# Kernel tuning notes

Hardware: AMD Instinct MI355X
Metric: run time of the kernel (lower is better)

## Reference

```python
import jax, jax.numpy as jnp
import numpy as np

B, S, V, D, L, H = 2, 512, 100300, 768, 12, 3072


def setup_inputs() -> dict:
    key = jax.random.key(0)
    ks = jax.random.split(key, 24)
    nrm = lambda k, shape, s=0.02: (jax.random.normal(k, shape, jnp.float32) * s)
    uni = lambda k, shape: jax.random.uniform(k, shape, jnp.float32)
    return {
        "tokens": jax.random.randint(ks[0], (B, S), 0, V, dtype=jnp.int32),
        "emb": nrm(ks[1], (V, D)),
        "ln0_g": jnp.ones((D,), jnp.float32), "ln0_b": jnp.zeros((D,), jnp.float32),
        "ln1_g": jnp.ones((L, D), jnp.float32), "ln1_b": jnp.zeros((L, D), jnp.float32),
        "ln2_g": jnp.ones((L, D), jnp.float32), "ln2_b": jnp.zeros((L, D), jnp.float32),
        "time_decay": nrm(ks[2], (L, D), 0.5),
        "time_first": nrm(ks[3], (L, D), 0.5),
        "tm_mu_k": uni(ks[4], (L, D)), "tm_mu_v": uni(ks[5], (L, D)), "tm_mu_r": uni(ks[6], (L, D)),
        "tm_Wk": nrm(ks[7], (L, D, D)), "tm_Wv": nrm(ks[8], (L, D, D)),
        "tm_Wr": nrm(ks[9], (L, D, D)), "tm_Wo": nrm(ks[10], (L, D, D)),
        "cm_mu_k": uni(ks[11], (L, D)), "cm_mu_r": uni(ks[12], (L, D)),
        "cm_Wk": nrm(ks[13], (L, D, H)), "cm_Wv": nrm(ks[14], (L, H, D)), "cm_Wr": nrm(ks[15], (L, D, D)),
        "lnf_g": jnp.ones((D,), jnp.float32), "lnf_b": jnp.zeros((D,), jnp.float32),
        "head": nrm(ks[16], (D, V)),
    }


def _ln(x, g, b, eps=1e-5):
    m = jnp.mean(x, axis=-1, keepdims=True)
    v = jnp.mean(jnp.square(x - m), axis=-1, keepdims=True)
    return (x - m) * jax.lax.rsqrt(v + eps) * g + b


def _shift(x):  # previous-token shift along seq axis, zeros at t=0; x: [B,S,D]
    return jnp.concatenate([jnp.zeros_like(x[:, :1]), x[:, :-1]], axis=1)


def _wkv(k, v, w, u):
    """RWKV-4 max-stabilized WKV linear recurrence. k,v: [B,S,D]; w,u: [D]."""
    decay = -jnp.exp(w)  # negative per-channel decay

    def step(carry, inp):
        p, a, b = carry
        kt, vt = inp
        ww = u + kt
        q = jnp.maximum(p, ww)
        e1 = jnp.exp(p - q)
        e2 = jnp.exp(ww - q)
        out = (e1 * a + e2 * vt) / (e1 * b + e2)
        ww2 = p + decay
        q2 = jnp.maximum(ww2, kt)
        e1 = jnp.exp(ww2 - q2)
        e2 = jnp.exp(kt - q2)
        return (q2, e1 * a + e2 * vt, e1 * b + e2), out

    kT = jnp.swapaxes(k, 0, 1)  # [S,B,D]
    vT = jnp.swapaxes(v, 0, 1)
    p0 = jnp.full((k.shape[0], k.shape[2]), -1e38, k.dtype)
    a0 = jnp.zeros_like(p0)
    b0 = jnp.zeros_like(p0)
    _, out = jax.lax.scan(step, (p0, a0, b0), (kT, vT))
    return jnp.swapaxes(out, 0, 1)  # [B,S,D]


def reference(tokens, emb, ln0_g, ln0_b, ln1_g, ln1_b, ln2_g, ln2_b,
              time_decay, time_first, tm_mu_k, tm_mu_v, tm_mu_r,
              tm_Wk, tm_Wv, tm_Wr, tm_Wo, cm_mu_k, cm_mu_r,
              cm_Wk, cm_Wv, cm_Wr, lnf_g, lnf_b, head):
    x = emb[tokens]                      # [B,S,D]
    x = _ln(x, ln0_g, ln0_b)
    n_layer = ln1_g.shape[0]
    for l in range(n_layer):
        # --- time mixing ---
        xx = _ln(x, ln1_g[l], ln1_b[l])
        sx = _shift(xx)
        xk = xx * tm_mu_k[l] + sx * (1.0 - tm_mu_k[l])
        xv = xx * tm_mu_v[l] + sx * (1.0 - tm_mu_v[l])
        xr = xx * tm_mu_r[l] + sx * (1.0 - tm_mu_r[l])
        r = jax.nn.sigmoid(jnp.einsum('bsd,de->bse', xr, tm_Wr[l]))
        k = jnp.einsum('bsd,de->bse', xk, tm_Wk[l])
        v = jnp.einsum('bsd,de->bse', xv, tm_Wv[l])
        wkv = _wkv(k, v, time_decay[l], time_first[l])
        x = x + jnp.einsum('bsd,de->bse', r * wkv, tm_Wo[l])
        # --- channel mixing ---
        xx = _ln(x, ln2_g[l], ln2_b[l])
        sx = _shift(xx)
        xk = xx * cm_mu_k[l] + sx * (1.0 - cm_mu_k[l])
        xr = xx * cm_mu_r[l] + sx * (1.0 - cm_mu_r[l])
        kk = jnp.square(jax.nn.relu(jnp.einsum('bsd,dh->bsh', xk, cm_Wk[l])))
        x = x + jax.nn.sigmoid(jnp.einsum('bsd,de->bse', xr, cm_Wr[l])) * jnp.einsum('bsh,hd->bsd', kk, cm_Wv[l])
    x = _ln(x, lnf_g, lnf_b)
    return jnp.einsum('bsd,dv->bsv', x, head)  # [B,S,V] logits
```

## Files before the change

### kernel.cpp

```cpp
#include <hip/hip_runtime.h>

typedef float f32x4v __attribute__((ext_vector_type(4)));
typedef __bf16 bf16x8 __attribute__((ext_vector_type(8)));

__device__ __forceinline__ ushort f2bf(float f) {
    unsigned u = __builtin_bit_cast(unsigned, f);
    return (ushort)((u + 0x7FFFu + ((u >> 16) & 1u)) >> 16);
}

__device__ __forceinline__ void gload16(const void* g, void* l) {
    __builtin_amdgcn_global_load_lds(
        (const __attribute__((address_space(1))) void*)g,
        (__attribute__((address_space(3))) void*)l, 16, 0, 0);
}

__global__ __launch_bounds__(256)
void prep_w(const float* __restrict__ Win, ushort* __restrict__ Wout,
            int K, int N, size_t sIn, size_t sOut)
{
    __shared__ float t[64][65];
    const float* W = Win + sIn * blockIdx.z;
    ushort* O = Wout + sOut * blockIdx.z;
    int n0 = blockIdx.x * 64, k0 = blockIdx.y * 64;
    int tid = threadIdx.x;
    int c = tid & 63, r4 = tid >> 6;
#pragma unroll
    for (int i = 0; i < 16; i++) {
        int rr = i * 4 + r4;
        int n = n0 + c;
        t[rr][c] = (n < N) ? W[(size_t)(k0 + rr) * N + n] : 0.f;
    }
    __syncthreads();
#pragma unroll
    for (int i = 0; i < 16; i++) {
        int nr = i * 4 + r4;
        O[(size_t)(n0 + nr) * K + k0 + c] = f2bf(t[c][nr]);
    }
}

__global__ __launch_bounds__(256)
void prep_dd(const float* __restrict__ W0, const float* __restrict__ W1,
             const float* __restrict__ W2, const float* __restrict__ W3,
             const float* __restrict__ W4,
             ushort* __restrict__ O0, ushort* __restrict__ O1,
             ushort* __restrict__ O2, ushort* __restrict__ O3,
             ushort* __restrict__ O4)
{
    __shared__ float t[64][65];
    const int z = blockIdx.z, wsel = z / 12, l = z % 12;
    const size_t DD = (size_t)768 * 768;
    const float* W = (wsel == 0 ? W0 : wsel == 1 ? W1 : wsel == 2 ? W2 : wsel == 3 ? W3 : W4) + DD * l;
    ushort* O = (wsel == 0 ? O0 : wsel == 1 ? O1 : wsel == 2 ? O2 : wsel == 3 ? O3 : O4) + DD * l;
    int n0 = blockIdx.x * 64, k0 = blockIdx.y * 64;
    int tid = threadIdx.x;
    int c = tid & 63, r4 = tid >> 6;
#pragma unroll
    for (int i = 0; i < 16; i++) {
        int rr = i * 4 + r4;
        t[rr][c] = W[(size_t)(k0 + rr) * 768 + n0 + c];
    }
    __syncthreads();
#pragma unroll
    for (int i = 0; i < 16; i++) {
        int nr = i * 4 + r4;
        O[(size_t)(n0 + nr) * 768 + k0 + c] = f2bf(t[c][nr]);
    }
}

template <int BM, int BN, int EPI>
__device__ __forceinline__
void gemm_body(const ushort* __restrict__ A, const ushort* __restrict__ B,
               float* __restrict__ C, ushort* __restrict__ Obf,
               const float* __restrict__ G,
               int N, int K, int mtiles, int bid, int tid,
               ushort* __restrict__ As, ushort* __restrict__ Bs)
{
    constexpr int WM = BM / 2, WN = BN / 2, MF = WM / 16, NF = WN / 16;
    const int mt = bid % mtiles, nt = bid / mtiles;
    const int m0 = mt * BM, n0 = nt * BN;
    const int w = tid >> 6, l = tid & 63;
    const int wr = w >> 1, wc = w & 1, g = l >> 4, lr = l & 15;
    const int lrow = l >> 3, lcol = ((l & 7) ^ lrow) * 8;

    auto stage = [&](int buf, int k0) {
#pragma unroll
        for (int i = 0; i < BM / 32; i++) {
            int rb = (i * 4 + w) * 8;
            gload16(A + (size_t)(m0 + rb + lrow) * K + k0 + lcol, &As[buf * BM * 64 + rb * 64]);
        }
#pragma unroll
        for (int i = 0; i < BN / 32; i++) {
            int rb = (i * 4 + w) * 8;
            gload16(B + (size_t)(n0 + rb + lrow) * K + k0 + lcol, &Bs[buf * BN * 64 + rb * 64]);
        }
    };

    f32x4v acc[MF][NF] = {};
    auto comp = [&](int buf) {
#pragma unroll
        for (int kk = 0; kk < 2; kk++) {
            bf16x8 af[MF], bfr[NF];
            const int sl = ((kk * 4 + g) ^ (lr & 7)) * 8;
#pragma unroll
            for (int mi = 0; mi < MF; mi++)
                af[mi] = *(const bf16x8*)&As[buf * BM * 64 + (wr * WM + mi * 16 + lr) * 64 + sl];
#pragma unroll
            for (int ni = 0; ni < NF; ni++)
                bfr[ni] = *(const bf16x8*)&Bs[buf * BN * 64 + (wc * WN + ni * 16 + lr) * 64 + sl];
#pragma unroll
            for (int mi = 0; mi < MF; mi++)
#pragma unroll
                for (int ni = 0; ni < NF; ni++)
                    acc[mi][ni] = __builtin_amdgcn_mfma_f32_16x16x32_bf16(
                        af[mi], bfr[ni], acc[mi][ni], 0, 0, 0);
        }
    };

    const int NS = K >> 6;
    stage(0, 0);
    __syncthreads();
    for (int s = 0; s < NS; s++) {
        if (s + 1 < NS) stage((s + 1) & 1, (s + 1) << 6);
        comp(s & 1);
        __syncthreads();
    }

#pragma unroll
    for (int mi = 0; mi < MF; mi++) {
        int row = m0 + wr * WM + mi * 16 + 4 * g;
#pragma unroll
        for (int ni = 0; ni < NF; ni++) {
            int col = n0 + wc * WN + ni * 16 + lr;
#pragma unroll
            for (int q = 0; q < 4; q++) {
                size_t idx = (size_t)(row + q) * N + col;
                float vv = acc[mi][ni][q];
                if constexpr (EPI == 0) {
                    C[idx] = vv;
                } else if constexpr (EPI == 1) {
                    C[idx] += vv;
                } else if constexpr (EPI == 2) {
                    float t = vv > 0.f ? vv : 0.f;
                    Obf[idx] = f2bf(t * t);
                } else {
                    float gt = 1.f / (1.f + __expf(-G[idx]));
                    C[idx] += gt * vv;
                }
            }
        }
    }
}

template <int BM, int BN, int EPI>
__global__ __launch_bounds__(256)
void gemm2(const ushort* __restrict__ Abase,
           const ushort* __restrict__ B0, const ushort* __restrict__ B1,
           const ushort* __restrict__ B2,
           float* __restrict__ Cbase, ushort* __restrict__ ObfBase,
           const float* __restrict__ Gbase,
           int M, int N, int K, int mtiles)
{
    __shared__ ushort As[2 * BM * 64];
    __shared__ ushort Bs[2 * BN * 64];
    const int z = blockIdx.z;
    const ushort* A = Abase + (size_t)z * M * K;
    const ushort* B = (z == 0) ? B0 : ((z == 1) ? B1 : B2);
    float* C = Cbase ? Cbase + (size_t)z * M * N : nullptr;
    ushort* Obf = ObfBase ? ObfBase + (size_t)z * M * N : nullptr;
    int bid = blockIdx.x;
    { int cpx = gridDim.x >> 3; bid = (bid & 7) * cpx + (bid >> 3); }
    gemm_body<BM, BN, EPI>(A, B, C, Obf, Gbase, N, K, mtiles, bid, threadIdx.x, As, Bs);
}

__global__ __launch_bounds__(256)
void gemm_ckcr(const ushort* __restrict__ xk, const ushort* __restrict__ xr,
               const ushort* __restrict__ ckT, const ushort* __restrict__ crT,
               ushort* __restrict__ hbuf, float* __restrict__ rrb)
{
    __shared__ ushort As[2 * 64 * 64];
    __shared__ ushort Bs[2 * 128 * 64];
    int bid = blockIdx.x;
    { int cpx = gridDim.x >> 3; bid = (bid & 7) * cpx + (bid >> 3); }
    if (bid < 384)
        gemm_body<64, 128, 2>(xk, ckT, nullptr, hbuf, nullptr, 3072, 768, 16,
                              bid, threadIdx.x, As, Bs);
    else
        gemm_body<64, 64, 0>(xr, crT, rrb, nullptr, nullptr, 768, 768, 16,
                             bid - 384, threadIdx.x, As, Bs);
}

__global__ __launch_bounds__(256, 4)
void head_gemm(const ushort* __restrict__ A, const ushort* __restrict__ B,
               float* __restrict__ C, int M, int N, int K, int mtiles)
{
    constexpr int WM = 64, WN = 64;
    __shared__ ushort As[2][128 * 32];
    __shared__ ushort Bs[2][128 * 32];

    int bid = blockIdx.x;
    { int cpx = gridDim.x >> 3; bid = (bid & 7) * cpx + (bid >> 3); }
    const int mt = bid % mtiles, nt = bid / mtiles;
    const int m0 = mt * 128, n0 = nt * 128;
    const int tid = threadIdx.x, w = tid >> 6, l = tid & 63;
    const int wr = w >> 1, wc = w & 1, g = l >> 4, lr = l & 15;
    const int lrow = l >> 2;
    const int lcol = ((l & 3) ^ (lrow & 3) ^ ((lrow >> 2) & 3)) * 8;

    auto stage = [&](int buf, int k0) {
#pragma unroll
        for (int i = 0; i < 2; i++) {
            int rg = i * 4 + w;
            gload16(A + (size_t)(m0 + rg * 16 + lrow) * K + k0 + lcol, &As[buf][rg * 512]);
        }
#pragma unroll
        for (int i = 0; i < 2; i++) {
            int rg = i * 4 + w;
            gload16(B + (size_t)(n0 + rg * 16 + lrow) * K + k0 + lcol, &Bs[buf][rg * 512]);
        }
    };

    f32x4v acc[4][4] = {};
    auto comp = [&](int buf) {
        bf16x8 af[4], bfr[4];
        const int sl = (g ^ (lr & 3) ^ ((lr >> 2) & 3)) * 8;
#pragma unroll
        for (int mi = 0; mi < 4; mi++)
            af[mi] = *(const bf16x8*)&As[buf][(wr * WM + mi * 16 + lr) * 32 + sl];
#pragma unroll
        for (int ni = 0; ni < 4; ni++)
            bfr[ni] = *(const bf16x8*)&Bs[buf][(wc * WN + ni * 16 + lr) * 32 + sl];
#pragma unroll
        for (int mi = 0; mi < 4; mi++)
#pragma unroll
            for (int ni = 0; ni < 4; ni++)
                acc[mi][ni] = __builtin_amdgcn_mfma_f32_16x16x32_bf16(
                    af[mi], bfr[ni], acc[mi][ni], 0, 0, 0);
    };

    const int NS = K / 32;
    stage(0, 0);
    __syncthreads();
    for (int s = 0; s < NS; s++) {
        if (s + 1 < NS) stage((s + 1) & 1, (s + 1) * 32);
        comp(s & 1);
        __syncthreads();
    }

#pragma unroll
    for (int mi = 0; mi < 4; mi++) {
        int row = m0 + wr * WM + mi * 16 + 4 * g;
#pragma unroll
        for (int ni = 0; ni < 4; ni++) {
            int col = n0 + wc * WN + ni * 16 + lr;
            if (col >= N) continue;
#pragma unroll
            for (int q = 0; q < 4; q++)
                C[(size_t)(row + q) * N + col] = acc[mi][ni][q];
        }
    }
}

__device__ __forceinline__ float4 blockReduce4(float4 v) {
#pragma unroll
    for (int off = 32; off; off >>= 1) {
        v.x += __shfl_down(v.x, off);
        v.y += __shfl_down(v.y, off);
        v.z += __shfl_down(v.z, off);
        v.w += __shfl_down(v.w, off);
    }
    __shared__ float4 red[4];
    int tid = threadIdx.x;
    if ((tid & 63) == 0) red[tid >> 6] = v;
    __syncthreads();
    float4 r = red[0];
    r.x += red[1].x + red[2].x + red[3].x;
    r.y += red[1].y + red[2].y + red[3].y;
    r.z += red[1].z + red[2].z + red[3].z;
    r.w += red[1].w + red[2].w + red[3].w;
    return r;
}

__global__ void embed_ln0(const int* __restrict__ tokens, const float* __restrict__ emb,
                          const float* __restrict__ g, const float* __restrict__ be,
                          float* __restrict__ x)
{
    int tau = blockIdx.x, tid = threadIdx.x;
    const float* e = emb + (size_t)tokens[tau] * 768;
    float a[3]; float s1 = 0, s2 = 0;
#pragma unroll
    for (int i = 0; i < 3; i++) {
        float av = e[tid + i * 256]; a[i] = av; s1 += av; s2 += av * av;
    }
    float4 r = blockReduce4(make_float4(s1, s2, 0.f, 0.f));
    const float inv = 1.f / 768.f;
    float m = r.x * inv, va = r.y * inv - m * m, rs = rsqrtf(va + 1e-5f);
#pragma unroll
    for (int i = 0; i < 3; i++) {
        int d = tid + i * 256;
        x[(size_t)tau * 768 + d] = (a[i] - m) * rs * g[d] + be[d];
    }
}

__global__ void ln_mix_tm(const float* __restrict__ x,
                          const float* __restrict__ g, const float* __restrict__ be,
                          const float* __restrict__ muk, const float* __restrict__ muv,
                          const float* __restrict__ mur,
                          ushort* __restrict__ xk, ushort* __restrict__ xv,
                          ushort* __restrict__ xr)
{
    int tau = blockIdx.x, tid = threadIdx.x;
    bool hasp = (tau & 511) != 0;
    const float* xp = x + (size_t)tau * 768;
    const float* pp = xp - 768;
    float a[3], b[3]; float s1 = 0, s2 = 0, s3 = 0, s4 = 0;
#pragma unroll
    for (int i = 0; i < 3; i++) {
        int d = tid + i * 256;
        float av = xp[d]; a[i] = av; s1 += av; s2 += av * av;
        float bv = hasp ? pp[d] : 0.f; b[i] = bv; s3 += bv; s4 += bv * bv;
    }
    float4 r = blockReduce4(make_float4(s1, s2, s3, s4));
    const float inv = 1.f / 768.f;
    float m1 = r.x * inv, va = r.y * inv - m1 * m1, rs1 = rsqrtf(va + 1e-5f);
    float m2 = r.z * inv, vb = r.w * inv - m2 * m2, rs2 = rsqrtf(vb + 1e-5f);
#pragma unroll
    for (int i = 0; i < 3; i++) {
        int d = tid + i * 256;
        float gg = g[d], bb = be[d];
        float xx = (a[i] - m1) * rs1 * gg + bb;
        float sx = hasp ? ((b[i] - m2) * rs2 * gg + bb) : 0.f;
        size_t o = (size_t)tau * 768 + d;
        float mk = muk[d]; xk[o] = f2bf(xx * mk + sx * (1.f - mk));
        float mv = muv[d]; xv[o] = f2bf(xx * mv + sx * (1.f - mv));
        float mr = mur[d]; xr[o] = f2bf(xx * mr + sx * (1.f - mr));
    }
}

__global__ void ln_mix_cm(const float* __restrict__ x,
                          const float* __restrict__ g, const float* __restrict__ be,
                          const float* __restrict__ muk, const float* __restrict__ mur,
                          ushort* __restrict__ xk, ushort* __restrict__ xr)
{
    int tau = blockIdx.x, tid = threadIdx.x;
    bool hasp = (tau & 511) != 0;
    const float* xp = x + (size_t)tau * 768;
    const float* pp = xp - 768;
    float a[3], b[3]; float s1 = 0, s2 = 0, s3 = 0, s4 = 0;
#pragma unroll
    for (int i = 0; i < 3; i++) {
        int d = tid + i * 256;
        float av = xp[d]; a[i] = av; s1 += av; s2 += av * av;
        float bv = hasp ? pp[d] : 0.f; b[i] = bv; s3 += bv; s4 += bv * bv;
    }
    float4 r = blockReduce4(make_float4(s1, s2, s3, s4));
    const float inv = 1.f / 768.f;
    float m1 = r.x * inv, va = r.y * inv - m1 * m1, rs1 = rsqrtf(va + 1e-5f);
    float m2 = r.z * inv, vb = r.w * inv - m2 * m2, rs2 = rsqrtf(vb + 1e-5f);
#pragma unroll
    for (int i = 0; i < 3; i++) {
        int d = tid + i * 256;
        float gg = g[d], bb = be[d];
        float xx = (a[i] - m1) * rs1 * gg + bb;
        float sx = hasp ? ((b[i] - m2) * rs2 * gg + bb) : 0.f;
        size_t o = (size_t)tau * 768 + d;
        float mk = muk[d]; xk[o] = f2bf(xx * mk + sx * (1.f - mk));
        float mr = mur[d]; xr[o] = f2bf(xx * mr + sx * (1.f - mr));
    }
}

__global__ void ln_final(const float* __restrict__ x,
                         const float* __restrict__ g, const float* __restrict__ be,
                         ushort* __restrict__ xf)
{
    int tau = blockIdx.x, tid = threadIdx.x;
    const float* xp = x + (size_t)tau * 768;
    float a[3]; float s1 = 0, s2 = 0;
#pragma unroll
    for (int i = 0; i < 3; i++) {
        float av = xp[tid + i * 256]; a[i] = av; s1 += av; s2 += av * av;
    }
    float4 r = blockReduce4(make_float4(s1, s2, 0.f, 0.f));
    const float inv = 1.f / 768.f;
    float m = r.x * inv, va = r.y * inv - m * m, rs = rsqrtf(va + 1e-5f);
#pragma unroll
    for (int i = 0; i < 3; i++) {
        int d = tid + i * 256;
        xf[(size_t)tau * 768 + d] = f2bf((a[i] - m) * rs * g[d] + be[d]);
    }
}

__global__ __launch_bounds__(256)
void wkv_par(const float* __restrict__ kk, const float* __restrict__ vv,
             const float* __restrict__ rr, const float* __restrict__ td,
             const float* __restrict__ tf, ushort* __restrict__ out)
{
    const int blk = blockIdx.x, tid = threadIdx.x;
    const int b = blk / 12, chb = blk % 12;
    const int seg = tid >> 6, ch = tid & 63;
    const int d = chb * 64 + ch;
    const size_t base = (size_t)b * 512 * 768 + d;
    const size_t soff = (size_t)seg * 128 * 768;
    const float w = -__expf(td[d]);
    const float u = tf[d];
    const int CH = 8;

    __shared__ float sp[192], sa[192], sb[192];
    __shared__ float pp[256], pa[256], pb[256];

    {
        float p = -1e38f, aa = 0.f, bb = 0.f;
        if (seg < 3) {
            const float* kp = kk + base + soff;
            const float* vp = vv + base + soff;
            float k8[CH], v8[CH], kn[CH], vn[CH];
#pragma unroll
            for (int j = 0; j < CH; j++) { k8[j] = kp[j * 768]; v8[j] = vp[j * 768]; }
            for (int c = 0; c < 128 / CH; c++) {
                if (c + 1 < 128 / CH) {
                    size_t o = (size_t)(c + 1) * CH * 768;
#pragma unroll
                    for (int j = 0; j < CH; j++) { kn[j] = kp[o + j * 768]; vn[j] = vp[o + j * 768]; }
                }
#pragma unroll
                for (int j = 0; j < CH; j++) {
                    float kt = k8[j], vt = v8[j];
                    float ww2 = p + w;
                    float q2 = fmaxf(ww2, kt);
                    float f1 = __expf(ww2 - q2), f2 = __expf(kt - q2);
                    aa = f1 * aa + f2 * vt;
                    bb = f1 * bb + f2;
                    p = q2;
                }
#pragma unroll
                for (int j = 0; j < CH; j++) { k8[j] = kn[j]; v8[j] = vn[j]; }
            }
            sp[seg * 64 + ch] = p; sa[seg * 64 + ch] = aa; sb[seg * 64 + ch] = bb;
        }
    }
    __syncthreads();

    if (tid < 64) {
        const float shift = 128.f * w;
        float P = -1e38f, A = 0.f, Bc = 0.f;
#pragma unroll
        for (int s = 0; s < 4; s++) {
            pp[s * 64 + tid] = P; pa[s * 64 + tid] = A; pb[s * 64 + tid] = Bc;
            if (s < 3) {
                float ps = P + shift;
                float sps = sp[s * 64 + tid];
                float q = fmaxf(ps, sps);
                float e1 = __expf(ps - q), e2 = __expf(sps - q);
                A  = e1 * A  + e2 * sa[s * 64 + tid];
                Bc = e1 * Bc + e2 * sb[s * 64 + tid];
                P = q;
            }
        }
    }
    __syncthreads();

    {
        float p = pp[tid], aa = pa[tid], bb = pb[tid];
        const float* kp = kk + base + soff;
        const float* vp = vv + base + soff;
        const float* rp = rr + base + soff;
        ushort* op = out + base + soff;
        float k8[CH], v8[CH], r8[CH], kn[CH], vn[CH], rn[CH];
#pragma unroll
        for (int j = 0; j < CH; j++) {
            k8[j] = kp[j * 768]; v8[j] = vp[j * 768]; r8[j] = rp[j * 768];
        }
        for (int c = 0; c < 128 / CH; c++) {
            if (c + 1 < 128 / CH) {
                size_t o = (size_t)(c + 1) * CH * 768;
#pragma unroll
                for (int j = 0; j < CH; j++) {
                    kn[j] = kp[o + j * 768]; vn[j] = vp[o + j * 768]; rn[j] = rp[o + j * 768];
                }
            }
#pragma unroll
            for (int j = 0; j < CH; j++) {
                float kt = k8[j], vt = v8[j];
                float ww = u + kt;
                float q = fmaxf(p, ww);
                float e1 = __expf(p - q), e2 = __expf(ww - q);
                float o = (e1 * aa + e2 * vt) / (e1 * bb + e2);
                float sr = 1.f / (1.f + __expf(-r8[j]));
                op[(size_t)(c * CH + j) * 768] = f2bf(sr * o);
                float ww2 = p + w;
                float q2 = fmaxf(ww2, kt);
                float f1 = __expf(ww2 - q2), f2 = __expf(kt - q2);
                aa = f1 * aa + f2 * vt;
                bb = f1 * bb + f2;
                p = q2;
            }
#pragma unroll
            for (int j = 0; j < CH; j++) { k8[j] = kn[j]; v8[j] = vn[j]; r8[j] = rn[j]; }
        }
    }
}

extern "C" void kernel_launch(void* const* d_in, const int* in_sizes, int n_in,
                              void* d_out, int out_size, void* d_ws, size_t ws_size,
                              hipStream_t stream)
{
    const int V = 100300, D = 768, L = 12, H = 3072;
    const int T = 1024;
    const int Vp = 100352;

    const int*   tokens     = (const int*)d_in[0];
    const float* emb        = (const float*)d_in[1];
    const float* ln0_g      = (const float*)d_in[2];
    const float* ln0_b      = (const float*)d_in[3];
    const float* ln1_g      = (const float*)d_in[4];
    const float* ln1_b      = (const float*)d_in[5];
    const float* ln2_g      = (const float*)d_in[6];
    const float* ln2_b      = (const float*)d_in[7];
    const float* time_decay = (const float*)d_in[8];
    const float* time_first = (const float*)d_in[9];
    const float* tm_mu_k    = (const float*)d_in[10];
    const float* tm_mu_v    = (const float*)d_in[11];
    const float* tm_mu_r    = (const float*)d_in[12];
    const float* tm_Wk      = (const float*)d_in[13];
    const float* tm_Wv      = (const float*)d_in[14];
    const float* tm_Wr      = (const float*)d_in[15];
    const float* tm_Wo      = (const float*)d_in[16];
    const float* cm_mu_k    = (const float*)d_in[17];
    const float* cm_mu_r    = (const float*)d_in[18];
    const float* cm_Wk      = (const float*)d_in[19];
    const float* cm_Wv      = (const float*)d_in[20];
    const float* cm_Wr      = (const float*)d_in[21];
    const float* lnf_g      = (const float*)d_in[22];
    const float* lnf_b      = (const float*)d_in[23];
    const float* head       = (const float*)d_in[24];

    char* wp = (char*)d_ws;
    auto alloc = [&](size_t bytes) -> char* {
        char* p = wp; wp += (bytes + 255) & ~(size_t)255; return p;
    };
    const size_t eDD = (size_t)L * D * D;
    const size_t eDH = (size_t)L * D * H;
    ushort* wkT = (ushort*)alloc(eDD * 2);
    ushort* wvT = (ushort*)alloc(eDD * 2);
    ushort* wrT = (ushort*)alloc(eDD * 2);
    ushort* woT = (ushort*)alloc(eDD * 2);
    ushort* ckT = (ushort*)alloc(eDH * 2);
    ushort* cvT = (ushort*)alloc(eDH * 2);
    ushort* crT = (ushort*)alloc(eDD * 2);
    ushort* hdT = (ushort*)alloc((size_t)Vp * D * 2);

    float*  x    = (float*)alloc((size_t)T * D * 4);
    ushort* xkb  = (ushort*)alloc((size_t)3 * T * D * 2);
    float*  kvr  = (float*)alloc((size_t)3 * T * D * 4);
    ushort* rwkv = (ushort*)alloc((size_t)T * D * 2);
    ushort* hbuf = (ushort*)alloc((size_t)T * H * 2);
    float*  rrb  = (float*)alloc((size_t)T * D * 4);
    ushort* xf   = (ushort*)alloc((size_t)T * D * 2);

    prep_dd<<<dim3(12, 12, 60), 256, 0, stream>>>(tm_Wk, tm_Wv, tm_Wr, tm_Wo, cm_Wr,
                                                  wkT, wvT, wrT, woT, crT);
    prep_w<<<dim3(H / 64, D / 64, L), 256, 0, stream>>>(cm_Wk, ckT, D, H, (size_t)D * H, (size_t)D * H);
    prep_w<<<dim3(D / 64, H / 64, L), 256, 0, stream>>>(cm_Wv, cvT, H, D, (size_t)D * H, (size_t)D * H);
    prep_w<<<dim3(Vp / 64, D / 64, 1), 256, 0, stream>>>(head, hdT, D, V, 0, 0);

    embed_ln0<<<T, 256, 0, stream>>>(tokens, emb, ln0_g, ln0_b, x);

    for (int l = 0; l < L; l++) {
        ln_mix_tm<<<T, 256, 0, stream>>>(x, ln1_g + l * D, ln1_b + l * D,
                                         tm_mu_k + l * D, tm_mu_v + l * D, tm_mu_r + l * D,
                                         xkb, xkb + (size_t)T * D, xkb + (size_t)2 * T * D);

        gemm2<64, 64, 0><<<dim3(192, 1, 3), 256, 0, stream>>>(
            xkb, wkT + l * (size_t)D * D, wvT + l * (size_t)D * D, wrT + l * (size_t)D * D,
            kvr, nullptr, nullptr, T, D, D, 16);

        wkv_par<<<24, 256, 0, stream>>>(kvr, kvr + (size_t)T * D, kvr + (size_t)2 * T * D,
                                        time_decay + l * D, time_first + l * D, rwkv);

        gemm2<64, 64, 1><<<dim3(192, 1, 1), 256, 0, stream>>>(
            rwkv, woT + l * (size_t)D * D, nullptr, nullptr,
            x, nullptr, nullptr, T, D, D, 16);

        ln_mix_cm<<<T, 256, 0, stream>>>(x, ln2_g + l * D, ln2_b + l * D,
                                         cm_mu_k + l * D, cm_mu_r + l * D,
                                         xkb, xkb + (size_t)T * D);

        gemm_ckcr<<<576, 256, 0, stream>>>(xkb, xkb + (size_t)T * D,
                                           ckT + l * (size_t)D * H, crT + l * (size_t)D * D,
                                           hbuf, rrb);

        gemm2<64, 64, 3><<<dim3(192, 1, 1), 256, 0, stream>>>(
            hbuf, cvT + l * (size_t)D * H, nullptr, nullptr,
            x, nullptr, rrb, T, D, H, 16);
    }

    ln_final<<<T, 256, 0, stream>>>(x, lnf_g, lnf_b, xf);

    head_gemm<<<8 * (Vp / 128), 256, 0, stream>>>(xf, hdT, (float*)d_out, T, V, D, 8);
}
```

Before: 2.134 ms.

## Restage head GEMM epilogue through LDS, new swizzle, and split WKV into eight segments

The head GEMM gets a new LDS swizzle layout for its operand tiles and a higher occupancy hint. Its output now goes through shared memory, so each thread writes coalesced float4 rows to the large logits matrix instead of scattered scalar stores. Separately, the WKV scan kernel splits the sequence into eight 64-step segments over 32 channels per block and doubles the grid to 48 blocks. This shortens the serial recurrence chain and uses more CUs, at the cost of a longer cross-segment combine and extra syncs in the GEMM epilogue.

```diff
diff --git a/kernel.cpp b/kernel.cpp
--- a/kernel.cpp
+++ b/kernel.cpp
@@ -189,13 +189,13 @@
                              bid - 384, threadIdx.x, As, Bs);
 }
 
-__global__ __launch_bounds__(256, 4)
+__global__ __launch_bounds__(256, 5)
 void head_gemm(const ushort* __restrict__ A, const ushort* __restrict__ B,
                float* __restrict__ C, int M, int N, int K, int mtiles)
 {
-    constexpr int WM = 64, WN = 64;
-    __shared__ ushort As[2][128 * 32];
-    __shared__ ushort Bs[2][128 * 32];
+    __shared__ ushort shm[16384];
+    ushort* As = shm;
+    ushort* Bs = shm + 8192;
 
     int bid = blockIdx.x;
     { int cpx = gridDim.x >> 3; bid = (bid & 7) * cpx + (bid >> 3); }
@@ -203,32 +203,43 @@
     const int m0 = mt * 128, n0 = nt * 128;
     const int tid = threadIdx.x, w = tid >> 6, l = tid & 63;
     const int wr = w >> 1, wc = w & 1, g = l >> 4, lr = l & 15;
-    const int lrow = l >> 2;
-    const int lcol = ((l & 3) ^ (lrow & 3) ^ ((lrow >> 2) & 3)) * 8;
 
     auto stage = [&](int buf, int k0) {
 #pragma unroll
         for (int i = 0; i < 2; i++) {
-            int rg = i * 4 + w;
-            gload16(A + (size_t)(m0 + rg * 16 + lrow) * K + k0 + lcol, &As[buf][rg * 512]);
+            int c = i * 256 + tid;
+            int P = c >> 3, s = c & 7, sp = s ^ (P & 7);
+            int row = 2 * P + (sp >> 2), ks = sp & 3;
+            gload16(A + (size_t)(m0 + row) * K + k0 + ks * 8,
+                    As + buf * 4096 + (i * 256 + (tid & 192)) * 8);
         }
 #pragma unroll
         for (int i = 0; i < 2; i++) {
-            int rg = i * 4 + w;
-            gload16(B + (size_t)(n0 + rg * 16 + lrow) * K + k0 + lcol, &Bs[buf][rg * 512]);
+            int c = i * 256 + tid;
+            int P = c >> 3, s = c & 7, sp = s ^ (P & 7);
+            int row = 2 * P + (sp >> 2), ks = sp & 3;
+            gload16(B + (size_t)(n0 + row) * K + k0 + ks * 8,
+                    Bs + buf * 4096 + (i * 256 + (tid & 192)) * 8);
         }
     };
 
     f32x4v acc[4][4] = {};
     auto comp = [&](int buf) {
         bf16x8 af[4], bfr[4];
-        const int sl = (g ^ (lr & 3) ^ ((lr >> 2) & 3)) * 8;
-#pragma unroll
-        for (int mi = 0; mi < 4; mi++)
-            af[mi] = *(const bf16x8*)&As[buf][(wr * WM + mi * 16 + lr) * 32 + sl];
-#pragma unroll
-        for (int ni = 0; ni < 4; ni++)
-            bfr[ni] = *(const bf16x8*)&Bs[buf][(wc * WN + ni * 16 + lr) * 32 + sl];
+#pragma unroll
+        for (int mi = 0; mi < 4; mi++) {
+            int row = wr * 64 + mi * 16 + lr;
+            int P = row >> 1;
+            int s = (((row & 1) << 2) | g) ^ (P & 7);
+            af[mi] = *(const bf16x8*)&As[buf * 4096 + P * 64 + s * 8];
+        }
+#pragma unroll
+        for (int ni = 0; ni < 4; ni++) {
+            int row = wc * 64 + ni * 16 + lr;
+            int P = row >> 1;
+            int s = (((row & 1) << 2) | g) ^ (P & 7);
+            bfr[ni] = *(const bf16x8*)&Bs[buf * 4096 + P * 64 + s * 8];
+        }
 #pragma unroll
         for (int mi = 0; mi < 4; mi++)
 #pragma unroll
@@ -246,16 +257,44 @@
         __syncthreads();
     }
 
-#pragma unroll
-    for (int mi = 0; mi < 4; mi++) {
-        int row = m0 + wr * WM + mi * 16 + 4 * g;
-#pragma unroll
-        for (int ni = 0; ni < 4; ni++) {
-            int col = n0 + wc * WN + ni * 16 + lr;
-            if (col >= N) continue;
-#pragma unroll
-            for (int q = 0; q < 4; q++)
-                C[(size_t)(row + q) * N + col] = acc[mi][ni][q];
+    __syncthreads();
+    float* fb = (float*)shm;
+#pragma unroll
+    for (int p = 0; p < 2; p++) {
+        if (p) __syncthreads();
+        if (wr == p) {
+#pragma unroll
+            for (int mi = 0; mi < 4; mi++)
+#pragma unroll
+                for (int ni = 0; ni < 4; ni++)
+#pragma unroll
+                    for (int q = 0; q < 4; q++) {
+                        int r = mi * 16 + 4 * g + q;
+                        int col = wc * 64 + ni * 16 + lr;
+                        fb[r * 128 + ((((col >> 2) ^ (r & 7)) << 2) | (col & 3))] =
+                            acc[mi][ni][q];
+                    }
+        }
+        __syncthreads();
+        const int rbase = m0 + p * 64;
+#pragma unroll
+        for (int sg = 0; sg < 4; sg++) {
+            int r = sg * 16 + (tid >> 4);
+            int grow = rbase + r;
+#pragma unroll
+            for (int i = 0; i < 2; i++) {
+                int j = (tid & 15) + 16 * i;
+                float4 v = *(const float4*)&fb[r * 128 + ((j ^ (r & 7)) << 2)];
+                int col = n0 + 4 * j;
+                if (col + 3 < N) {
+                    *(float4*)&C[(size_t)grow * N + col] = v;
+                } else {
+                    const float* pv = &v.x;
+#pragma unroll
+                    for (int e = 0; e < 4; e++)
+                        if (col + e < N) C[(size_t)grow * N + col + e] = pv[e];
+                }
+            }
         }
     }
 }
@@ -395,63 +434,61 @@
              const float* __restrict__ tf, ushort* __restrict__ out)
 {
     const int blk = blockIdx.x, tid = threadIdx.x;
-    const int b = blk / 12, chb = blk % 12;
-    const int seg = tid >> 6, ch = tid & 63;
-    const int d = chb * 64 + ch;
+    const int b = blk / 24, chb = blk % 24;
+    const int seg = tid >> 5, ch = tid & 31;
+    const int d = chb * 32 + ch;
     const size_t base = (size_t)b * 512 * 768 + d;
-    const size_t soff = (size_t)seg * 128 * 768;
+    const size_t soff = (size_t)seg * 64 * 768;
     const float w = -__expf(td[d]);
     const float u = tf[d];
     const int CH = 8;
 
-    __shared__ float sp[192], sa[192], sb[192];
+    __shared__ float sp[224], sa[224], sb[224];
     __shared__ float pp[256], pa[256], pb[256];
 
-    {
+    if (seg < 7) {
         float p = -1e38f, aa = 0.f, bb = 0.f;
-        if (seg < 3) {
-            const float* kp = kk + base + soff;
-            const float* vp = vv + base + soff;
-            float k8[CH], v8[CH], kn[CH], vn[CH];
-#pragma unroll
-            for (int j = 0; j < CH; j++) { k8[j] = kp[j * 768]; v8[j] = vp[j * 768]; }
-            for (int c = 0; c < 128 / CH; c++) {
-                if (c + 1 < 128 / CH) {
-                    size_t o = (size_t)(c + 1) * CH * 768;
-#pragma unroll
-                    for (int j = 0; j < CH; j++) { kn[j] = kp[o + j * 768]; vn[j] = vp[o + j * 768]; }
-                }
-#pragma unroll
-                for (int j = 0; j < CH; j++) {
-                    float kt = k8[j], vt = v8[j];
-                    float ww2 = p + w;
-                    float q2 = fmaxf(ww2, kt);
-                    float f1 = __expf(ww2 - q2), f2 = __expf(kt - q2);
-                    aa = f1 * aa + f2 * vt;
-                    bb = f1 * bb + f2;
-                    p = q2;
-                }
-#pragma unroll
-                for (int j = 0; j < CH; j++) { k8[j] = kn[j]; v8[j] = vn[j]; }
+        const float* kp = kk + base + soff;
+        const float* vp = vv + base + soff;
+        float k8[CH], v8[CH], kn[CH], vn[CH];
+#pragma unroll
+        for (int j = 0; j < CH; j++) { k8[j] = kp[j * 768]; v8[j] = vp[j * 768]; }
+        for (int c = 0; c < 64 / CH; c++) {
+            if (c + 1 < 64 / CH) {
+                size_t o = (size_t)(c + 1) * CH * 768;
+#pragma unroll
+                for (int j = 0; j < CH; j++) { kn[j] = kp[o + j * 768]; vn[j] = vp[o + j * 768]; }
             }
-            sp[seg * 64 + ch] = p; sa[seg * 64 + ch] = aa; sb[seg * 64 + ch] = bb;
-        }
-    }
-    __syncthreads();
-
-    if (tid < 64) {
-        const float shift = 128.f * w;
+#pragma unroll
+            for (int j = 0; j < CH; j++) {
+                float kt = k8[j], vt = v8[j];
+                float ww2 = p + w;
+                float q2 = fmaxf(ww2, kt);
+                float f1 = __expf(ww2 - q2), f2 = __expf(kt - q2);
+                aa = f1 * aa + f2 * vt;
+                bb = f1 * bb + f2;
+                p = q2;
+            }
+#pragma unroll
+            for (int j = 0; j < CH; j++) { k8[j] = kn[j]; v8[j] = vn[j]; }
+        }
+        sp[seg * 32 + ch] = p; sa[seg * 32 + ch] = aa; sb[seg * 32 + ch] = bb;
+    }
+    __syncthreads();
+
+    if (tid < 32) {
+        const float shift = 64.f * w;
         float P = -1e38f, A = 0.f, Bc = 0.f;
 #pragma unroll
-        for (int s = 0; s < 4; s++) {
-            pp[s * 64 + tid] = P; pa[s * 64 + tid] = A; pb[s * 64 + tid] = Bc;
-            if (s < 3) {
+        for (int s = 0; s < 8; s++) {
+            pp[s * 32 + tid] = P; pa[s * 32 + tid] = A; pb[s * 32 + tid] = Bc;
+            if (s < 7) {
                 float ps = P + shift;
-                float sps = sp[s * 64 + tid];
+                float sps = sp[s * 32 + tid];
                 float q = fmaxf(ps, sps);
                 float e1 = __expf(ps - q), e2 = __expf(sps - q);
-                A  = e1 * A  + e2 * sa[s * 64 + tid];
-                Bc = e1 * Bc + e2 * sb[s * 64 + tid];
+                A  = e1 * A  + e2 * sa[s * 32 + tid];
+                Bc = e1 * Bc + e2 * sb[s * 32 + tid];
                 P = q;
             }
         }
@@ -469,8 +506,8 @@
         for (int j = 0; j < CH; j++) {
             k8[j] = kp[j * 768]; v8[j] = vp[j * 768]; r8[j] = rp[j * 768];
         }
-        for (int c = 0; c < 128 / CH; c++) {
-            if (c + 1 < 128 / CH) {
+        for (int c = 0; c < 64 / CH; c++) {
+            if (c + 1 < 64 / CH) {
                 size_t o = (size_t)(c + 1) * CH * 768;
 #pragma unroll
                 for (int j = 0; j < CH; j++) {
@@ -573,7 +610,7 @@
             xkb, wkT + l * (size_t)D * D, wvT + l * (size_t)D * D, wrT + l * (size_t)D * D,
             kvr, nullptr, nullptr, T, D, D, 16);
 
-        wkv_par<<<24, 256, 0, stream>>>(kvr, kvr + (size_t)T * D, kvr + (size_t)2 * T * D,
+        wkv_par<<<48, 256, 0, stream>>>(kvr, kvr + (size_t)T * D, kvr + (size_t)2 * T * D,
                                         time_decay + l * D, time_first + l * D, rwkv);
 
         gemm2<64, 64, 1><<<dim3(192, 1, 1), 256, 0, stream>>>(
```

Result: faster. 2.054 ms (-3.7%).
